# Kernel tuning notes

Measured on AMD Instinct MI355X. Metric: run time of the kernel, lower is better.

## Reference

```python
import jax, jax.numpy as jnp
import numpy as np

NUM_EMBEDDINGS = 1024
EMBEDDING_DIM = 64
COMMITMENT_COST = 0.25
EPS_NORM = 1e-12  # torch F.normalize eps


def _l2_normalize(x):
    n = jnp.linalg.norm(x, axis=-1, keepdims=True)
    return x / jnp.maximum(n, EPS_NORM)


def setup_inputs() -> dict:
    key = jax.random.key(0)
    k1, k2 = jax.random.split(key)
    inputs = jax.random.normal(k1, (16, 4096, EMBEDDING_DIM), dtype=jnp.float32)
    weight = jax.random.normal(k2, (NUM_EMBEDDINGS, EMBEDDING_DIM), dtype=jnp.float32) * 0.02
    return {"inputs": inputs, "weight": weight}


def reference(inputs, weight):
    input_shape = inputs.shape
    x = _l2_normalize(inputs)                      # [B,S,D]
    flat = x.reshape(-1, EMBEDDING_DIM)            # [N,D]
    w = _l2_normalize(weight)                      # [K,D]

    distances = (jnp.sum(flat ** 2, axis=1, keepdims=True)
                 + jnp.sum(w ** 2, axis=1)
                 - 2.0 * flat @ w.T)               # [N,K]
    encoding_indices = jnp.argmin(distances, axis=1)  # [N]

    quantized = w[encoding_indices].reshape(input_shape)  # [B,S,D]

    e_latent_loss = jnp.mean((jax.lax.stop_gradient(quantized) - x) ** 2)
    q_latent_loss = jnp.mean((quantized - jax.lax.stop_gradient(x)) ** 2)
    loss = q_latent_loss + COMMITMENT_COST * e_latent_loss

    # straight-through estimator
    quantized_ste = x + jax.lax.stop_gradient(quantized - x)

    # perplexity (no-grad bookkeeping)
    n = encoding_indices.shape[0]
    counts = jnp.zeros((NUM_EMBEDDINGS,), jnp.float32).at[encoding_indices].add(1.0)
    avg_probs = counts / n
    perplexity = jnp.exp(-jnp.sum(avg_probs * jnp.log(avg_probs + 1e-10)))

    return loss, quantized_ste, perplexity, encoding_indices[:, None]
```

## Files before the change

### kernel.cpp

```cpp
#include <hip/hip_runtime.h>
#include <hip/hip_bf16.h>
#include <math.h>

#define NROWS   65536
#define DIM     64
#define KCODES  1024
#define RPB     128
#define TPB     512
#define NBLOCKS (NROWS / RPB)

#define NEXACT 9u

typedef short short8 __attribute__((ext_vector_type(8)));
typedef float f32x4  __attribute__((ext_vector_type(4)));

#define OUT_Q_OFF    ((size_t)1)
#define OUT_PERP_OFF ((size_t)(1 + (size_t)NROWS * DIM))
#define OUT_IDX_OFF  ((size_t)(2 + (size_t)NROWS * DIM))

#define WS_COUNTS 0
#define WS_SSEC   4096
#define WS_DONE   4100
#define WS_WN     8192
#define WS_SK     (WS_WN + KCODES*DIM*4)
#define WS_WNH    (WS_SK + KCODES*4)
#define WS_WNL    (WS_WNH + KCODES*DIM*2)

__device__ __forceinline__ unsigned short bf16_rne(float f) {
  unsigned u = __float_as_uint(f);
  return (unsigned short)((u + 0x7FFFu + ((u >> 16) & 1u)) >> 16);
}
__device__ __forceinline__ float bf16f(unsigned short h) {
  return __uint_as_float(((unsigned)h) << 16);
}
__device__ __forceinline__ unsigned med3u(unsigned a, unsigned b, unsigned c) {
  unsigned d;
  asm("v_med3_u32 %0, %1, %2, %3" : "=v"(d) : "v"(a), "v"(b), "v"(c));
  return d;
}
__device__ __forceinline__ unsigned uminu(unsigned a, unsigned b) { return a < b ? a : b; }
__device__ __forceinline__ unsigned umaxu(unsigned a, unsigned b) { return a > b ? a : b; }

__global__ void __launch_bounds__(64) normalize_w_kernel(
    const float* __restrict__ w, float* __restrict__ wn, float* __restrict__ sk,
    unsigned short* __restrict__ wnh, unsigned short* __restrict__ wnl,
    unsigned* __restrict__ counts, float* __restrict__ sse_accum,
    unsigned* __restrict__ done) {
  const int k = blockIdx.x;
  const int d = threadIdx.x;
  if (d == 0) {
    counts[k] = 0u;
    if (k == 0) { *sse_accum = 0.f; *done = 0u; }
  }
  float v = w[k * DIM + d];
  float ss = v * v;
  #pragma unroll
  for (int o = 32; o > 0; o >>= 1) ss += __shfl_xor(ss, o, 64);
  const float den = fmaxf(sqrtf(ss), 1e-12f);
  const float q = v / den;
  wn[k * DIM + d] = q;
  const unsigned short h = bf16_rne(q);
  wnh[k * DIM + d] = h;
  wnl[k * DIM + d] = bf16_rne(q - bf16f(h));
  float s2 = q * q;
  #pragma unroll
  for (int o = 32; o > 0; o >>= 1) s2 += __shfl_xor(s2, o, 64);
  if (d == 0) sk[k] = s2;
}

__global__ void __launch_bounds__(TPB, 4) vq_mega_kernel(
    const float* __restrict__ x, const unsigned short* __restrict__ wnh,
    const unsigned short* __restrict__ wnl, const float* __restrict__ sk,
    const float* __restrict__ wn, float* __restrict__ out,
    unsigned* __restrict__ counts, float* __restrict__ sse_accum,
    unsigned* __restrict__ done) {
  __shared__ __align__(16) unsigned AB[9216];
  __shared__ float skb[2][64];
  __shared__ float c_arr[RPB];
  __shared__ float rowsse[RPB];
  __shared__ int   ib[RPB];
  __shared__ int   qlist[RPB];
  __shared__ int   flist[RPB];
  __shared__ int   qn_s, fn_s;
  __shared__ int   islast;
  __shared__ float hred[8];
  const int tid = threadIdx.x;
  const int lane = tid & 63, wave = tid >> 6;
  const int rg = wave >> 1, cg = wave & 1;

  if (tid == 0) { qn_s = 0; fn_s = 0; }

  {
    const int row_l = tid >> 2;
    const int qr = tid & 3;
    const size_t row = (size_t)blockIdx.x * RPB + row_l;
    const float4* xr = (const float4*)(x + row * DIM) + qr * 4;
    float4 xv[4];
    float ss = 0.f;
    #pragma unroll
    for (int i = 0; i < 4; i++) {
      xv[i] = xr[i];
      ss += xv[i].x * xv[i].x + xv[i].y * xv[i].y + xv[i].z * xv[i].z + xv[i].w * xv[i].w;
    }
    ss += __shfl_xor(ss, 1, 64); ss += __shfl_xor(ss, 2, 64);
    const float inv = 1.0f / fmaxf(sqrtf(ss), 1e-12f);
    float c = 0.f;
    #pragma unroll
    for (int i = 0; i < 4; i++) {
      const float a0 = xv[i].x * inv, a1 = xv[i].y * inv;
      const float a2 = xv[i].z * inv, a3 = xv[i].w * inv;
      c += a0 * a0 + a1 * a1 + a2 * a2 + a3 * a3;
      const unsigned short h0 = bf16_rne(a0), h1 = bf16_rne(a1);
      const unsigned short h2 = bf16_rne(a2), h3 = bf16_rne(a3);
      const unsigned short l0 = bf16_rne(a0 - bf16f(h0)), l1 = bf16_rne(a1 - bf16f(h1));
      const unsigned short l2 = bf16_rne(a2 - bf16f(h2)), l3 = bf16_rne(a3 - bf16f(h3));
      AB[row_l * 36 + qr * 8 + 2 * i]            = (unsigned)h0 | ((unsigned)h1 << 16);
      AB[row_l * 36 + qr * 8 + 2 * i + 1]        = (unsigned)h2 | ((unsigned)h3 << 16);
      AB[4608 + row_l * 36 + qr * 8 + 2 * i]     = (unsigned)l0 | ((unsigned)l1 << 16);
      AB[4608 + row_l * 36 + qr * 8 + 2 * i + 1] = (unsigned)l2 | ((unsigned)l3 << 16);
    }
    c += __shfl_xor(c, 1, 64); c += __shfl_xor(c, 2, 64);
    if (qr == 0) c_arr[row_l] = c;
  }
  __syncthreads();

  short8 ah[2][2], al[2][2];
  #pragma unroll
  for (int rt = 0; rt < 2; rt++)
    #pragma unroll
    for (int kk = 0; kk < 2; kk++) {
      const int r = rg * 32 + rt * 16 + (lane & 15);
      ah[rt][kk] = *(const short8*)&AB[r * 36 + kk * 16 + (lane >> 4) * 4];
      al[rt][kk] = *(const short8*)&AB[4608 + r * 36 + kk * 16 + (lane >> 4) * 4];
    }
  __syncthreads();

  unsigned k1[8], k2[8], k3[8];
  #pragma unroll
  for (int s = 0; s < 8; s++) { k1[s] = 0xFFFFFFFFu; k2[s] = 0xFFFFFFFFu; k3[s] = 0xFFFFFFFFu; }

  {
    const int code = tid >> 3, q = tid & 7;
    *(float4*)&AB[code * 36 + q * 4]        = *(const float4*)(wnh + (size_t)code * DIM + q * 8);
    *(float4*)&AB[2304 + code * 36 + q * 4] = *(const float4*)(wnl + (size_t)code * DIM + q * 8);
    if (tid < 64) skb[0][tid] = sk[tid] + 4.0f;
  }

  #pragma unroll 2
  for (int c = 0; c < 16; c++) {
    const int b = c & 1;
    __syncthreads();
    if (c < 15) {
      const int nb = b ^ 1;
      const int code = tid >> 3, q = tid & 7;
      *(float4*)&AB[nb * 4608 + code * 36 + q * 4] =
          *(const float4*)(wnh + (size_t)((c + 1) * 64 + code) * DIM + q * 8);
      *(float4*)&AB[nb * 4608 + 2304 + code * 36 + q * 4] =
          *(const float4*)(wnl + (size_t)((c + 1) * 64 + code) * DIM + q * 8);
      if (tid < 64) skb[nb][tid] = sk[(c + 1) * 64 + tid] + 4.0f;
    }
    #pragma unroll
    for (int tt = 0; tt < 2; tt++) {
      const int cb = cg * 32 + tt * 16 + (lane & 15);
      const float skv4 = skb[b][cb];
      const unsigned chi = (unsigned)(c * 4 + cg * 2 + tt);
      const short8 bh0 = *(const short8*)&AB[b * 4608 + cb * 36 + 0 * 16 + (lane >> 4) * 4];
      const short8 bh1 = *(const short8*)&AB[b * 4608 + cb * 36 + 1 * 16 + (lane >> 4) * 4];
      const short8 bl0 = *(const short8*)&AB[b * 4608 + 2304 + cb * 36 + 0 * 16 + (lane >> 4) * 4];
      const short8 bl1 = *(const short8*)&AB[b * 4608 + 2304 + cb * 36 + 1 * 16 + (lane >> 4) * 4];
      #pragma unroll
      for (int rt = 0; rt < 2; rt++) {
        f32x4 acc = {0.f, 0.f, 0.f, 0.f};
        acc = __builtin_amdgcn_mfma_f32_16x16x32_bf16(ah[rt][0], bh0, acc, 0, 0, 0);
        acc = __builtin_amdgcn_mfma_f32_16x16x32_bf16(ah[rt][1], bh1, acc, 0, 0, 0);
        acc = __builtin_amdgcn_mfma_f32_16x16x32_bf16(al[rt][0], bh0, acc, 0, 0, 0);
        acc = __builtin_amdgcn_mfma_f32_16x16x32_bf16(al[rt][1], bh1, acc, 0, 0, 0);
        acc = __builtin_amdgcn_mfma_f32_16x16x32_bf16(ah[rt][0], bl0, acc, 0, 0, 0);
        acc = __builtin_amdgcn_mfma_f32_16x16x32_bf16(ah[rt][1], bl1, acc, 0, 0, 0);
        #pragma unroll
        for (int i = 0; i < 4; i++) {
          const float dist4 = fmaf(-2.0f, acc[i], skv4);
          const unsigned key = (__float_as_uint(dist4) & 0xFFFFFFC0u) | chi;
          const int s = rt * 4 + i;
          const unsigned t = umaxu(k1[s], key);
          k3[s] = med3u(k2[s], k3[s], t);
          k2[s] = med3u(k1[s], k2[s], key);
          k1[s] = uminu(k1[s], key);
        }
      }
    }
  }

  #pragma unroll
  for (int s = 0; s < 8; s++) {
    unsigned a1 = (k1[s] << 4) | (unsigned)(lane & 15);
    unsigned a2 = (k2[s] << 4) | (unsigned)(lane & 15);
    unsigned a3 = (k3[s] << 4) | (unsigned)(lane & 15);
    #pragma unroll
    for (int m = 1; m < 16; m <<= 1) {
      const unsigned p1 = (unsigned)__shfl_xor((int)a1, m, 64);
      const unsigned p2 = (unsigned)__shfl_xor((int)a2, m, 64);
      const unsigned p3 = (unsigned)__shfl_xor((int)a3, m, 64);
      const unsigned th = umaxu(a1, p1);
      const unsigned n1 = uminu(a1, p1);
      const unsigned m2 = uminu(a2, p2);
      const unsigned m3 = uminu(a3, p3);
      const unsigned hi = umaxu(th, m2);
      a1 = n1;
      a2 = uminu(th, m2);
      a3 = uminu(hi, med3u(th, m2, m3));
    }
    if ((lane & 15) == 0) {
      const int row_local = rg * 32 + (s >> 2) * 16 + (lane >> 4) * 4 + (s & 3);
      AB[cg * 384 + row_local * 3 + 0] = a1;
      AB[cg * 384 + row_local * 3 + 1] = a2;
      AB[cg * 384 + row_local * 3 + 2] = a3;
    }
  }
  __syncthreads();

  if (tid < RPB) {
    const unsigned x1 = AB[tid * 3 + 0], x2 = AB[tid * 3 + 1], x3 = AB[tid * 3 + 2];
    const unsigned y1 = AB[384 + tid * 3 + 0], y2 = AB[384 + tid * 3 + 1],
                   y3 = AB[384 + tid * 3 + 2];
    const unsigned m1 = uminu(x1, y1);
    const unsigned t1 = umaxu(x1, y1);
    const unsigned u  = uminu(x2, y2);
    const unsigned m2 = uminu(t1, u);
    const unsigned m3 = med3u(t1, u, uminu(umaxu(x2, y2), uminu(x3, y3)));
    const int i1 = (int)(m1 & 1023u);
    ib[tid] = i1;
    const unsigned ub = ((m1 & 0xFFFFFC00u) >> 4) | 0x40000000u;
    rowsse[tid] = __uint_as_float(ub) - 4.0f + c_arr[tid] + 1.6e-5f;
    const unsigned b1 = m1 >> 10, b2 = m2 >> 10, b3 = m3 >> 10;
    if (b3 - b1 < NEXACT) {
      flist[atomicAdd(&fn_s, 1)] = tid;
    } else if (b2 - b1 < NEXACT) {
      qlist[atomicAdd(&qn_s, 1)] = tid | (i1 << 7) | ((int)(m2 & 1023u) << 17);
    }
  }
  __syncthreads();

  const int qn = qn_s, fn = fn_s;
  if (tid < qn) {
    const int packed = qlist[tid];
    const int rl = packed & 127;
    const int c1 = (packed >> 7) & 1023, c2i = (packed >> 17) & 1023;
    const size_t row = (size_t)blockIdx.x * RPB + rl;
    const float4* xr = (const float4*)(x + row * DIM);
    float4 xv[16];
    float ss = 0.f;
    #pragma unroll
    for (int i = 0; i < 16; i++) {
      xv[i] = xr[i];
      ss += xv[i].x * xv[i].x + xv[i].y * xv[i].y + xv[i].z * xv[i].z + xv[i].w * xv[i].w;
    }
    const float den = fmaxf(sqrtf(ss), 1e-12f);
    #pragma unroll
    for (int i = 0; i < 16; i++) { xv[i].x /= den; xv[i].y /= den; xv[i].z /= den; xv[i].w /= den; }
    float cc = 0.f;
    #pragma unroll
    for (int i = 0; i < 16; i++)
      cc += xv[i].x * xv[i].x + xv[i].y * xv[i].y + xv[i].z * xv[i].z + xv[i].w * xv[i].w;
    float dd[2]; const int cand[2] = {c1, c2i};
    #pragma unroll
    for (int t = 0; t < 2; t++) {
      const float4* wr = (const float4*)(wn + (size_t)cand[t] * DIM);
      float e0 = 0.f, e1 = 0.f, e2 = 0.f, e3 = 0.f;
      #pragma unroll
      for (int i = 0; i < 16; i++) {
        const float4 wv = wr[i];
        e0 = fmaf(xv[i].x, wv.x, e0);
        e1 = fmaf(xv[i].y, wv.y, e1);
        e2 = fmaf(xv[i].z, wv.z, e2);
        e3 = fmaf(xv[i].w, wv.w, e3);
      }
      dd[t] = (cc + sk[cand[t]]) - 2.0f * ((e0 + e1) + (e2 + e3));
    }
    const bool tb = (dd[1] < dd[0]) || (dd[1] == dd[0] && c2i < c1);
    ib[rl] = tb ? c2i : c1;
    rowsse[rl] = tb ? dd[1] : dd[0];
  }

  for (int qi = wave; qi < fn; qi += 8) {
    const int rl = flist[qi];
    const size_t row = (size_t)blockIdx.x * RPB + rl;
    const float4* xr = (const float4*)(x + row * DIM);
    float4 xv[16];
    float ss = 0.f;
    #pragma unroll
    for (int i = 0; i < 16; i++) {
      xv[i] = xr[i];
      ss += xv[i].x * xv[i].x + xv[i].y * xv[i].y + xv[i].z * xv[i].z + xv[i].w * xv[i].w;
    }
    const float den = fmaxf(sqrtf(ss), 1e-12f);
    #pragma unroll
    for (int i = 0; i < 16; i++) { xv[i].x /= den; xv[i].y /= den; xv[i].z /= den; xv[i].w /= den; }
    float cc = 0.f;
    #pragma unroll
    for (int i = 0; i < 16; i++)
      cc += xv[i].x * xv[i].x + xv[i].y * xv[i].y + xv[i].z * xv[i].z + xv[i].w * xv[i].w;

    float best = INFINITY;
    int bidx = 0x7FFFFFFF;
    for (int j = 0; j < 16; j++) {
      const int k = j * 64 + lane;
      const float4* wr = (const float4*)(wn + (size_t)k * DIM);
      float e0 = 0.f, e1 = 0.f, e2 = 0.f, e3 = 0.f;
      #pragma unroll
      for (int i = 0; i < 16; i++) {
        const float4 wv = wr[i];
        e0 = fmaf(xv[i].x, wv.x, e0);
        e1 = fmaf(xv[i].y, wv.y, e1);
        e2 = fmaf(xv[i].z, wv.z, e2);
        e3 = fmaf(xv[i].w, wv.w, e3);
      }
      const float dot = (e0 + e1) + (e2 + e3);
      const float dist = (cc + sk[k]) - 2.0f * dot;
      if (dist < best) { best = dist; bidx = k; }
    }
    #pragma unroll
    for (int m = 1; m < 64; m <<= 1) {
      const float pb = __shfl_xor(best, m, 64);
      const int pi = __shfl_xor(bidx, m, 64);
      if (pb < best || (pb == best && pi < bidx)) { best = pb; bidx = pi; }
    }
    if (lane == 0) { ib[rl] = bidx; rowsse[rl] = best; }
  }
  __syncthreads();

  if (tid < RPB) {
    const size_t row = (size_t)blockIdx.x * RPB + tid;
    const int idx = ib[tid];
    out[OUT_IDX_OFF + row] = (float)idx;
    atomicAdd(&counts[idx], 1u);
  }

  const size_t obase = OUT_Q_OFF + (size_t)blockIdx.x * (RPB * DIM);
  #pragma unroll 4
  for (int j = 0; j < 16; j++) {
    const int e = j * TPB + tid;
    out[obase + e] = wn[(size_t)ib[e >> 6] * DIM + (e & 63)];
  }

  __syncthreads();
  for (int s = 64; s > 0; s >>= 1) {
    if (tid < s) rowsse[tid] += rowsse[tid + s];
    __syncthreads();
  }
  if (tid == 0) atomicAdd(sse_accum, rowsse[0]);

  if (tid == 0) {
    __threadfence();
    islast = (atomicAdd(done, 1u) == NBLOCKS - 1) ? 1 : 0;
  }
  __syncthreads();
  if (islast) {
    __threadfence();
    float h = 0.f;
    #pragma unroll
    for (int i = 0; i < 2; i++) {
      const float cv = (float)counts[tid * 2 + i];
      const float avg = cv * (1.0f / (float)NROWS);
      h += avg * logf(avg + 1e-10f);
    }
    #pragma unroll
    for (int o = 32; o > 0; o >>= 1) h += __shfl_xor(h, o, 64);
    if (lane == 0) hred[wave] = h;
    __syncthreads();
    if (tid == 0) {
      const float H = -(hred[0] + hred[1] + hred[2] + hred[3] +
                        hred[4] + hred[5] + hred[6] + hred[7]);
      const float mse = *sse_accum * (1.0f / (float)((size_t)NROWS * DIM));
      out[0] = mse + 0.25f * mse;
      out[OUT_PERP_OFF] = expf(H);
    }
  }
}

extern "C" void kernel_launch(void* const* d_in, const int* in_sizes, int n_in,
                              void* d_out, int out_size, void* d_ws, size_t ws_size,
                              hipStream_t stream) {
  const float* x = (const float*)d_in[0];
  const float* w = (const float*)d_in[1];
  float* out = (float*)d_out;

  char* ws = (char*)d_ws;
  unsigned* counts    = (unsigned*)(ws + WS_COUNTS);
  float* sse_accum    = (float*)(ws + WS_SSEC);
  unsigned* done      = (unsigned*)(ws + WS_DONE);
  float* wn           = (float*)(ws + WS_WN);
  float* sk           = (float*)(ws + WS_SK);
  unsigned short* wnh = (unsigned short*)(ws + WS_WNH);
  unsigned short* wnl = (unsigned short*)(ws + WS_WNL);

  normalize_w_kernel<<<KCODES, 64, 0, stream>>>(w, wn, sk, wnh, wnl,
                                                counts, sse_accum, done);
  vq_mega_kernel<<<NBLOCKS, TPB, 0, stream>>>(
      x, wnh, wnl, sk, wn, out, counts, sse_accum, done);
}
```

Baseline: 132.4 us.

## Keep codebook slice in registers per wave and stream rows from LDS

Each of the 8 waves now owns a fixed 128-code slice of the bf16 hi/lo codebook, loaded once from global memory into registers. It then loops over all 128 rows, reading the A fragments from LDS. This removes the double-buffered LDS streaming of the codebook and the per-chunk block barriers. Per-wave top-3 results go into a new 8-way shared TRI buffer and are merged by 128 threads. The trade-off is much higher register pressure, with launch bounds lowered from 4 to 2 blocks per SM, which reduces occupancy and latency hiding.

```diff
diff --git a/kernel.cpp b/kernel.cpp
--- a/kernel.cpp
+++ b/kernel.cpp
@@ -68,14 +68,14 @@
   if (d == 0) sk[k] = s2;
 }
 
-__global__ void __launch_bounds__(TPB, 4) vq_mega_kernel(
+__global__ void __launch_bounds__(TPB, 2) vq_mega_kernel(
     const float* __restrict__ x, const unsigned short* __restrict__ wnh,
     const unsigned short* __restrict__ wnl, const float* __restrict__ sk,
     const float* __restrict__ wn, float* __restrict__ out,
     unsigned* __restrict__ counts, float* __restrict__ sse_accum,
     unsigned* __restrict__ done) {
   __shared__ __align__(16) unsigned AB[9216];
-  __shared__ float skb[2][64];
+  __shared__ unsigned TRI[8 * RPB * 3];
   __shared__ float c_arr[RPB];
   __shared__ float rowsse[RPB];
   __shared__ int   ib[RPB];
@@ -86,9 +86,22 @@
   __shared__ float hred[8];
   const int tid = threadIdx.x;
   const int lane = tid & 63, wave = tid >> 6;
-  const int rg = wave >> 1, cg = wave & 1;
+  const int cg = wave;
 
   if (tid == 0) { qn_s = 0; fn_s = 0; }
+
+  short8 bh[8][2], bl[8][2];
+  float  skr[8];
+  #pragma unroll
+  for (int g = 0; g < 8; g++) {
+    const int code = cg * 128 + g * 16 + (lane & 15);
+    #pragma unroll
+    for (int kk = 0; kk < 2; kk++) {
+      bh[g][kk] = *(const short8*)(wnh + (size_t)code * DIM + kk * 32 + (lane >> 4) * 8);
+      bl[g][kk] = *(const short8*)(wnl + (size_t)code * DIM + kk * 32 + (lane >> 4) * 8);
+    }
+    skr[g] = sk[code] + 4.0f;
+  }
 
   {
     const int row_l = tid >> 2;
@@ -124,119 +137,89 @@
   }
   __syncthreads();
 
-  short8 ah[2][2], al[2][2];
-  #pragma unroll
-  for (int rt = 0; rt < 2; rt++)
-    #pragma unroll
-    for (int kk = 0; kk < 2; kk++) {
-      const int r = rg * 32 + rt * 16 + (lane & 15);
-      ah[rt][kk] = *(const short8*)&AB[r * 36 + kk * 16 + (lane >> 4) * 4];
-      al[rt][kk] = *(const short8*)&AB[4608 + r * 36 + kk * 16 + (lane >> 4) * 4];
-    }
-  __syncthreads();
-
-  unsigned k1[8], k2[8], k3[8];
-  #pragma unroll
-  for (int s = 0; s < 8; s++) { k1[s] = 0xFFFFFFFFu; k2[s] = 0xFFFFFFFFu; k3[s] = 0xFFFFFFFFu; }
-
-  {
-    const int code = tid >> 3, q = tid & 7;
-    *(float4*)&AB[code * 36 + q * 4]        = *(const float4*)(wnh + (size_t)code * DIM + q * 8);
-    *(float4*)&AB[2304 + code * 36 + q * 4] = *(const float4*)(wnl + (size_t)code * DIM + q * 8);
-    if (tid < 64) skb[0][tid] = sk[tid] + 4.0f;
-  }
-
-  #pragma unroll 2
-  for (int c = 0; c < 16; c++) {
-    const int b = c & 1;
-    __syncthreads();
-    if (c < 15) {
-      const int nb = b ^ 1;
-      const int code = tid >> 3, q = tid & 7;
-      *(float4*)&AB[nb * 4608 + code * 36 + q * 4] =
-          *(const float4*)(wnh + (size_t)((c + 1) * 64 + code) * DIM + q * 8);
-      *(float4*)&AB[nb * 4608 + 2304 + code * 36 + q * 4] =
-          *(const float4*)(wnl + (size_t)((c + 1) * 64 + code) * DIM + q * 8);
-      if (tid < 64) skb[nb][tid] = sk[(c + 1) * 64 + tid] + 4.0f;
-    }
-    #pragma unroll
-    for (int tt = 0; tt < 2; tt++) {
-      const int cb = cg * 32 + tt * 16 + (lane & 15);
-      const float skv4 = skb[b][cb];
-      const unsigned chi = (unsigned)(c * 4 + cg * 2 + tt);
-      const short8 bh0 = *(const short8*)&AB[b * 4608 + cb * 36 + 0 * 16 + (lane >> 4) * 4];
-      const short8 bh1 = *(const short8*)&AB[b * 4608 + cb * 36 + 1 * 16 + (lane >> 4) * 4];
-      const short8 bl0 = *(const short8*)&AB[b * 4608 + 2304 + cb * 36 + 0 * 16 + (lane >> 4) * 4];
-      const short8 bl1 = *(const short8*)&AB[b * 4608 + 2304 + cb * 36 + 1 * 16 + (lane >> 4) * 4];
+  for (int t = 0; t < 8; t++) {
+    const int r = t * 16 + (lane & 15);
+    const short8 ah0 = *(const short8*)&AB[r * 36 + 0 * 16 + (lane >> 4) * 4];
+    const short8 ah1 = *(const short8*)&AB[r * 36 + 1 * 16 + (lane >> 4) * 4];
+    const short8 al0 = *(const short8*)&AB[4608 + r * 36 + 0 * 16 + (lane >> 4) * 4];
+    const short8 al1 = *(const short8*)&AB[4608 + r * 36 + 1 * 16 + (lane >> 4) * 4];
+
+    unsigned k1[4], k2[4], k3[4];
+    #pragma unroll
+    for (int i = 0; i < 4; i++) { k1[i] = 0xFFFFFFFFu; k2[i] = 0xFFFFFFFFu; k3[i] = 0xFFFFFFFFu; }
+
+    #pragma unroll
+    for (int g = 0; g < 8; g++) {
+      f32x4 acc = {0.f, 0.f, 0.f, 0.f};
+      acc = __builtin_amdgcn_mfma_f32_16x16x32_bf16(ah0, bh[g][0], acc, 0, 0, 0);
+      acc = __builtin_amdgcn_mfma_f32_16x16x32_bf16(ah1, bh[g][1], acc, 0, 0, 0);
+      acc = __builtin_amdgcn_mfma_f32_16x16x32_bf16(al0, bh[g][0], acc, 0, 0, 0);
+      acc = __builtin_amdgcn_mfma_f32_16x16x32_bf16(al1, bh[g][1], acc, 0, 0, 0);
+      acc = __builtin_amdgcn_mfma_f32_16x16x32_bf16(ah0, bl[g][0], acc, 0, 0, 0);
+      acc = __builtin_amdgcn_mfma_f32_16x16x32_bf16(ah1, bl[g][1], acc, 0, 0, 0);
+      const unsigned chi = (unsigned)(cg * 8 + g);
       #pragma unroll
-      for (int rt = 0; rt < 2; rt++) {
-        f32x4 acc = {0.f, 0.f, 0.f, 0.f};
-        acc = __builtin_amdgcn_mfma_f32_16x16x32_bf16(ah[rt][0], bh0, acc, 0, 0, 0);
-        acc = __builtin_amdgcn_mfma_f32_16x16x32_bf16(ah[rt][1], bh1, acc, 0, 0, 0);
-        acc = __builtin_amdgcn_mfma_f32_16x16x32_bf16(al[rt][0], bh0, acc, 0, 0, 0);
-        acc = __builtin_amdgcn_mfma_f32_16x16x32_bf16(al[rt][1], bh1, acc, 0, 0, 0);
-        acc = __builtin_amdgcn_mfma_f32_16x16x32_bf16(ah[rt][0], bl0, acc, 0, 0, 0);
-        acc = __builtin_amdgcn_mfma_f32_16x16x32_bf16(ah[rt][1], bl1, acc, 0, 0, 0);
-        #pragma unroll
-        for (int i = 0; i < 4; i++) {
-          const float dist4 = fmaf(-2.0f, acc[i], skv4);
-          const unsigned key = (__float_as_uint(dist4) & 0xFFFFFFC0u) | chi;
-          const int s = rt * 4 + i;
-          const unsigned t = umaxu(k1[s], key);
-          k3[s] = med3u(k2[s], k3[s], t);
-          k2[s] = med3u(k1[s], k2[s], key);
-          k1[s] = uminu(k1[s], key);
-        }
-      }
-    }
-  }
-
-  #pragma unroll
-  for (int s = 0; s < 8; s++) {
-    unsigned a1 = (k1[s] << 4) | (unsigned)(lane & 15);
-    unsigned a2 = (k2[s] << 4) | (unsigned)(lane & 15);
-    unsigned a3 = (k3[s] << 4) | (unsigned)(lane & 15);
-    #pragma unroll
-    for (int m = 1; m < 16; m <<= 1) {
-      const unsigned p1 = (unsigned)__shfl_xor((int)a1, m, 64);
-      const unsigned p2 = (unsigned)__shfl_xor((int)a2, m, 64);
-      const unsigned p3 = (unsigned)__shfl_xor((int)a3, m, 64);
-      const unsigned th = umaxu(a1, p1);
-      const unsigned n1 = uminu(a1, p1);
-      const unsigned m2 = uminu(a2, p2);
-      const unsigned m3 = uminu(a3, p3);
-      const unsigned hi = umaxu(th, m2);
-      a1 = n1;
-      a2 = uminu(th, m2);
-      a3 = uminu(hi, med3u(th, m2, m3));
-    }
-    if ((lane & 15) == 0) {
-      const int row_local = rg * 32 + (s >> 2) * 16 + (lane >> 4) * 4 + (s & 3);
-      AB[cg * 384 + row_local * 3 + 0] = a1;
-      AB[cg * 384 + row_local * 3 + 1] = a2;
-      AB[cg * 384 + row_local * 3 + 2] = a3;
+      for (int i = 0; i < 4; i++) {
+        const float dist4 = fmaf(-2.0f, acc[i], skr[g]);
+        const unsigned key = (__float_as_uint(dist4) & 0xFFFFFFC0u) | chi;
+        const unsigned tt = umaxu(k1[i], key);
+        k3[i] = med3u(k2[i], k3[i], tt);
+        k2[i] = med3u(k1[i], k2[i], key);
+        k1[i] = uminu(k1[i], key);
+      }
+    }
+
+    #pragma unroll
+    for (int i = 0; i < 4; i++) {
+      unsigned a1 = (k1[i] << 4) | (unsigned)(lane & 15);
+      unsigned a2 = (k2[i] << 4) | (unsigned)(lane & 15);
+      unsigned a3 = (k3[i] << 4) | (unsigned)(lane & 15);
+      #pragma unroll
+      for (int m = 1; m < 16; m <<= 1) {
+        const unsigned p1 = (unsigned)__shfl_xor((int)a1, m, 64);
+        const unsigned p2 = (unsigned)__shfl_xor((int)a2, m, 64);
+        const unsigned p3 = (unsigned)__shfl_xor((int)a3, m, 64);
+        const unsigned th = umaxu(a1, p1);
+        a1 = uminu(a1, p1);
+        const unsigned m2 = uminu(a2, p2);
+        const unsigned m3 = uminu(a3, p3);
+        const unsigned hi = umaxu(th, m2);
+        a2 = uminu(th, m2);
+        a3 = uminu(hi, med3u(th, m2, m3));
+      }
+      if ((lane & 15) == 0) {
+        const int row_local = t * 16 + (lane >> 4) * 4 + i;
+        TRI[(cg * RPB + row_local) * 3 + 0] = a1;
+        TRI[(cg * RPB + row_local) * 3 + 1] = a2;
+        TRI[(cg * RPB + row_local) * 3 + 2] = a3;
+      }
     }
   }
   __syncthreads();
 
   if (tid < RPB) {
-    const unsigned x1 = AB[tid * 3 + 0], x2 = AB[tid * 3 + 1], x3 = AB[tid * 3 + 2];
-    const unsigned y1 = AB[384 + tid * 3 + 0], y2 = AB[384 + tid * 3 + 1],
-                   y3 = AB[384 + tid * 3 + 2];
-    const unsigned m1 = uminu(x1, y1);
-    const unsigned t1 = umaxu(x1, y1);
-    const unsigned u  = uminu(x2, y2);
-    const unsigned m2 = uminu(t1, u);
-    const unsigned m3 = med3u(t1, u, uminu(umaxu(x2, y2), uminu(x3, y3)));
-    const int i1 = (int)(m1 & 1023u);
+    unsigned a1 = TRI[tid * 3 + 0], a2 = TRI[tid * 3 + 1], a3 = TRI[tid * 3 + 2];
+    #pragma unroll
+    for (int w = 1; w < 8; w++) {
+      const unsigned b1 = TRI[(w * RPB + tid) * 3 + 0];
+      const unsigned b2 = TRI[(w * RPB + tid) * 3 + 1];
+      const unsigned b3 = TRI[(w * RPB + tid) * 3 + 2];
+      const unsigned t1 = umaxu(a1, b1);
+      const unsigned u  = uminu(a2, b2);
+      const unsigned n3 = med3u(t1, u, uminu(umaxu(a2, b2), uminu(a3, b3)));
+      a1 = uminu(a1, b1);
+      a2 = uminu(t1, u);
+      a3 = n3;
+    }
+    const int i1 = (int)(a1 & 1023u);
     ib[tid] = i1;
-    const unsigned ub = ((m1 & 0xFFFFFC00u) >> 4) | 0x40000000u;
+    const unsigned ub = ((a1 & 0xFFFFFC00u) >> 4) | 0x40000000u;
     rowsse[tid] = __uint_as_float(ub) - 4.0f + c_arr[tid] + 1.6e-5f;
-    const unsigned b1 = m1 >> 10, b2 = m2 >> 10, b3 = m3 >> 10;
+    const unsigned b1 = a1 >> 10, b2 = a2 >> 10, b3 = a3 >> 10;
     if (b3 - b1 < NEXACT) {
       flist[atomicAdd(&fn_s, 1)] = tid;
     } else if (b2 - b1 < NEXACT) {
-      qlist[atomicAdd(&qn_s, 1)] = tid | (i1 << 7) | ((int)(m2 & 1023u) << 17);
+      qlist[atomicAdd(&qn_s, 1)] = tid | (i1 << 7) | ((int)(a2 & 1023u) << 17);
     }
   }
   __syncthreads();
```

After: 147.6 us. 1.11x slower.
